# Kernel optimization log

Hardware: AMD Instinct MI355X
Metric: run time of the kernel (lower is better)

## Reference

```python
import jax, jax.numpy as jnp
import numpy as np

VOCAB = 16000   # code_size
EMBED = 16
HID = 256
B, T = 64, 128


def _glorot(key, shape, fan):
    return jax.random.normal(key, shape, dtype=jnp.float32) / np.sqrt(fan)


def setup_inputs() -> dict:
    key = jax.random.key(0)
    ks = jax.random.split(key, 20)
    inp = {
        "tokens": jax.random.randint(ks[0], (B, T), 0, VOCAB),
        "h0": jax.random.normal(ks[1], (B, HID), dtype=jnp.float32),
        "c0": jax.random.normal(ks[2], (B, HID), dtype=jnp.float32),
        "emb": jax.random.normal(ks[3], (VOCAB, EMBED), dtype=jnp.float32),
        # LSTMCell params, PyTorch layout: W_ih [4H, in], W_hh [4H, H], biases [4H]
        "Wih1": _glorot(ks[4], (4 * HID, EMBED), EMBED),
        "Whh1": _glorot(ks[5], (4 * HID, HID), HID),
        "bih1": jnp.zeros((4 * HID,), jnp.float32),
        "bhh1": jnp.zeros((4 * HID,), jnp.float32),
        "Wih2": _glorot(ks[6], (4 * HID, HID), HID),
        "Whh2": _glorot(ks[7], (4 * HID, HID), HID),
        "bih2": jnp.zeros((4 * HID,), jnp.float32),
        "bhh2": jnp.zeros((4 * HID,), jnp.float32),
        "Wih3": _glorot(ks[8], (4 * HID, HID), HID),
        "Whh3": _glorot(ks[9], (4 * HID, HID), HID),
        "bih3": jnp.zeros((4 * HID,), jnp.float32),
        "bhh3": jnp.zeros((4 * HID,), jnp.float32),
        # head: Linear(HID,HID) -> ReLU -> Linear(HID,VOCAB)
        "W1": _glorot(ks[10], (HID, HID), HID),
        "b1": jnp.zeros((HID,), jnp.float32),
        "W2": _glorot(ks[11], (VOCAB, HID), HID),
        "b2": jnp.zeros((VOCAB,), jnp.float32),
    }
    return inp


def _lstm_cell(x, h, c, Wih, Whh, bih, bhh):
    # PyTorch LSTMCell gate order: i, f, g, o
    gates = x @ Wih.T + bih + h @ Whh.T + bhh          # [B, 4H]
    i, f, g, o = jnp.split(gates, 4, axis=-1)
    i, f, o = jax.nn.sigmoid(i), jax.nn.sigmoid(f), jax.nn.sigmoid(o)
    g = jnp.tanh(g)
    c_new = f * c + i * g
    h_new = o * jnp.tanh(c_new)
    return h_new, c_new


def reference(tokens, h0, c0, emb,
              Wih1, Whh1, bih1, bhh1,
              Wih2, Whh2, bih2, bhh2,
              Wih3, Whh3, bih3, bhh3,
              W1, b1, W2, b2):
    Bn, Tn = tokens.shape
    x = emb[tokens]                       # [B, T, E]
    xs = jnp.swapaxes(x, 0, 1)            # [T, B, E] for scan over time

    def step(carry, x_t):
        h1, c1, h2, c2, h3, c3 = carry
        h1, c1 = _lstm_cell(x_t, h1, c1, Wih1, Whh1, bih1, bhh1)
        h2, c2 = _lstm_cell(h1, h2, c2, Wih2, Whh2, bih2, bhh2)
        h3, c3 = _lstm_cell(h2, h3, c3, Wih3, Whh3, bih3, bhh3)
        score = jax.nn.relu(h3 @ W1.T + b1) @ W2.T + b2   # [B, V]
        return (h1, c1, h2, c2, h3, c3), score

    init = (h0, c0, h0, c0, h0, c0)       # hidden1 = hidden2 = hidden3 = hidden
    _, scores = jax.lax.scan(step, init, xs)              # [T, B, V]
    scores = jnp.swapaxes(scores, 0, 1).reshape(Bn * Tn, -1)
    labels = tokens.reshape(-1)
    return scores, labels
```

## Files before the change

kernel.cpp:

```cpp
#include <hip/hip_runtime.h>
#include <hip/hip_bf16.h>
#include <stdint.h>

#define T_SEQ 128
#define BATCH 64
#define HIDN  256
#define EMB   16
#define VOCAB 16000

typedef __attribute__((ext_vector_type(8))) short short8v;
typedef __attribute__((ext_vector_type(4))) float f32x4;
typedef __attribute__((ext_vector_type(4))) unsigned short us4v;
typedef unsigned short ushort_t;
typedef unsigned long long u64_t;

#define OFF_WC1    0
#define OFF_WC2    131072
#define OFF_WC3    393216
#define OFF_BS2    655360
#define OFF_BS3    656384
#define OFF_FLAGS  657408
#define OFF_W1T    658432
#define OFF_H3     723968
#define OFF_S1     2821120
#define OFF_W2BF   3869696

#define OUT_XG     0
#define OUT_RINGS  8388608

#define RING_STRIDE 2113536
#define SLOT 16384

__device__ __forceinline__ ushort_t f2bf(float x) {
    __hip_bfloat16 h = __float2bfloat16(x);
    return *reinterpret_cast<ushort_t*>(&h);
}

__device__ __forceinline__ f32x4 sig4(f32x4 x) {
    f32x4 r;
    r[0] = __builtin_amdgcn_rcpf(1.f + __expf(-x[0]));
    r[1] = __builtin_amdgcn_rcpf(1.f + __expf(-x[1]));
    r[2] = __builtin_amdgcn_rcpf(1.f + __expf(-x[2]));
    r[3] = __builtin_amdgcn_rcpf(1.f + __expf(-x[3]));
    return r;
}
__device__ __forceinline__ f32x4 tanh4(f32x4 x) {
    f32x4 r;
    r[0] = 1.f - 2.f * __builtin_amdgcn_rcpf(1.f + __expf(2.f * x[0]));
    r[1] = 1.f - 2.f * __builtin_amdgcn_rcpf(1.f + __expf(2.f * x[1]));
    r[2] = 1.f - 2.f * __builtin_amdgcn_rcpf(1.f + __expf(2.f * x[2]));
    r[3] = 1.f - 2.f * __builtin_amdgcn_rcpf(1.f + __expf(2.f * x[3]));
    return r;
}
__device__ __forceinline__ f32x4 sx4(f32x4 v, int m) {
    f32x4 r;
    r[0] = __shfl_xor(v[0], m); r[1] = __shfl_xor(v[1], m);
    r[2] = __shfl_xor(v[2], m); r[3] = __shfl_xor(v[3], m);
    return r;
}
__device__ __forceinline__ void spin_ge(const int* p, int target) {
    while (__hip_atomic_load(p, __ATOMIC_RELAXED, __HIP_MEMORY_SCOPE_AGENT) < target) {}
}

__global__ void k_reset_flags(float* wsf) {
    ((int*)(wsf + OFF_FLAGS))[threadIdx.x] = 0;
}

__global__ void k_reorder_w(const float* __restrict__ Whh1,
                            const float* __restrict__ Wih2, const float* __restrict__ Whh2,
                            const float* __restrict__ Wih3, const float* __restrict__ Whh3,
                            float* __restrict__ wsf) {
    int bid = blockIdx.x;
    int layer = bid >> 10, c = bid & 1023;
    int wgi = c >> 7, rr = c & 127, jl = rr >> 2, gg = rr & 3;
    int row = gg * 256 + wgi * 32 + jl;
    int tid = threadIdx.x;
    if (layer == 0) {
        ushort_t* dst = (ushort_t*)(wsf + OFF_WC1) + (size_t)c * 256;
        dst[tid] = f2bf(Whh1[row * 256 + tid]);
    } else {
        const float* Wi = (layer == 1) ? Wih2 : Wih3;
        const float* Wh = (layer == 1) ? Whh2 : Whh3;
        ushort_t* dst = (ushort_t*)(wsf + ((layer == 1) ? OFF_WC2 : OFF_WC3)) + (size_t)c * 512;
        for (int k = tid; k < 512; k += 256)
            dst[k] = f2bf(k < 256 ? Wi[row * 256 + k] : Wh[row * 256 + k - 256]);
    }
}

__global__ void k_bias23(const float* __restrict__ bi2, const float* __restrict__ bh2,
                         const float* __restrict__ bi3, const float* __restrict__ bh3,
                         float* __restrict__ wsf) {
    int idx = blockIdx.x * 256 + threadIdx.x;
    int layer = idx >> 10, c = idx & 1023;
    int wgi = c >> 7, rr = c & 127, jl = rr >> 2, gg = rr & 3;
    int row = gg * 256 + wgi * 32 + jl;
    wsf[((layer == 0) ? OFF_BS2 : OFF_BS3) + c] =
        (layer == 0) ? (bi2[row] + bh2[row]) : (bi3[row] + bh3[row]);
}

__global__ void k_xg(const int* __restrict__ tokens, const float* __restrict__ emb,
                     const float* __restrict__ Wih1, const float* __restrict__ bih1,
                     const float* __restrict__ bhh1, float* __restrict__ xg) {
    int t = blockIdx.x, cg = blockIdx.y;
    int tid = threadIdx.x;
    __shared__ float xs[64][16];
    for (int idx = tid; idx < 1024; idx += 256) {
        int b = idx >> 4, e = idx & 15;
        xs[b][e] = emb[(size_t)tokens[b * T_SEQ + t] * 16 + e];
    }
    __syncthreads();
    int c = cg * 64 + (tid & 63);
    int b0 = (tid >> 6) * 16;
    int wgi = c >> 7, rr = c & 127, jl = rr >> 2, gg = rr & 3;
    int row = gg * 256 + wgi * 32 + jl;
    float wv[16];
    #pragma unroll
    for (int e = 0; e < 16; ++e) wv[e] = Wih1[row * 16 + e];
    float bias = bih1[row] + bhh1[row];
    float* dst = xg + ((size_t)t * 1024 + c) * 64 + b0;
    for (int b = 0; b < 16; ++b) {
        float s = bias;
        #pragma unroll
        for (int e = 0; e < 16; ++e) s += xs[b0 + b][e] * wv[e];
        dst[b] = s;
    }
}

__global__ void k_init_rings(const float* __restrict__ h0, ushort_t* __restrict__ rbase) {
    int idx = blockIdx.x * 256 + threadIdx.x;
    ushort_t v = f2bf(h0[idx]);
    rbase[idx] = v;
    rbase[RING_STRIDE + idx] = v;
    rbase[2 * RING_STRIDE + idx] = v;
}

__global__ void k_transpose_w1(const float* __restrict__ src, float* __restrict__ dst) {
    int idx = blockIdx.x * 256 + threadIdx.x;
    int n = idx & 255, k = idx >> 8;
    dst[idx] = src[n * 256 + k];
}

__global__ void k_conv_w2(const float* __restrict__ src, ushort_t* __restrict__ dst, int n) {
    int idx = blockIdx.x * 256 + threadIdx.x;
    if (idx < n) dst[idx] = f2bf(src[idx]);
}

template<int LAYER, int NKS>
__device__ __forceinline__ void lstm_body(
    int wg, int tid, const float* __restrict__ c0,
    float* __restrict__ wsf, float* __restrict__ outf,
    ushort_t* hA, ushort_t* hB, ushort_t* hS) {
    const int w = tid >> 6, lane = tid & 63, lr = lane & 15, lg = lane >> 4;
    const int g = lr & 3;
    const int K = NKS * 32;
    const ushort_t* WC = (const ushort_t*)(wsf + (LAYER == 0 ? OFF_WC1 : LAYER == 1 ? OFF_WC2 : OFF_WC3));
    int* fl = (int*)(wsf + OFF_FLAGS);
    float* H3 = wsf + OFF_H3;
    const float* xg = outf + OUT_XG;
    ushort_t* rbase = (ushort_t*)(outf + OUT_RINGS);
    ushort_t* ringIn = rbase + (size_t)(LAYER == 0 ? 0 : LAYER - 1) * RING_STRIDE;
    ushort_t* ringOwn = rbase + (size_t)LAYER * RING_STRIDE;

    const int ccol = wg * 128 + 2 * w * 16 + lr;
    short8v wr0[NKS], wr1[NKS];
    #pragma unroll
    for (int ks = 0; ks < NKS; ++ks) {
        wr0[ks] = *(const short8v*)(WC + (size_t)ccol * K + ks * 32 + lg * 8);
        wr1[ks] = *(const short8v*)(WC + (size_t)(ccol + 16) * K + ks * 32 + lg * 8);
    }
    float bs0 = 0.f, bs1 = 0.f;
    if (LAYER > 0) {
        const float* BS = wsf + (LAYER == 1 ? OFF_BS2 : OFF_BS3);
        bs0 = BS[ccol]; bs1 = BS[ccol + 16];
    }
    const int jj0 = w * 8 + (lr >> 2);
    const int j0 = wg * 32 + jj0;
    f32x4 cst[4][2];
    #pragma unroll
    for (int i = 0; i < 4; ++i)
        #pragma unroll
        for (int r = 0; r < 4; ++r) {
            cst[i][0][r] = c0[(i * 16 + lg * 4 + r) * 256 + j0];
            cst[i][1][r] = c0[(i * 16 + lg * 4 + r) * 256 + j0 + 4];
        }

    for (int t = 0; t < T_SEQ; ++t) {
        f32x4 xpre[8];
        if (LAYER == 0) {
            const float* xt = xg + ((size_t)t * 1024 + wg * 128) * 64;
            #pragma unroll
            for (int i = 0; i < 4; ++i) {
                xpre[i]     = *(const f32x4*)(xt + (size_t)(2 * w * 16 + lr) * 64 + i * 16 + lg * 4);
                xpre[i + 4] = *(const f32x4*)(xt + (size_t)((2 * w + 1) * 16 + lr) * 64 + i * 16 + lg * 4);
            }
        }
        if (LAYER == 0) {
            if (tid < 8) spin_ge(&fl[tid], t);
        } else {
            if (tid < 16) {
                int idx = tid & 7;
                const int* p = (tid < 8) ? &fl[(LAYER - 1) * 8 + idx] : &fl[LAYER * 8 + idx];
                spin_ge(p, (tid < 8) ? t + 1 : t);
            }
        }
        __syncthreads();
        {
            const u64_t* sA = (const u64_t*)(LAYER == 0 ? (ringOwn + (size_t)t * SLOT)
                                                        : (ringIn + (size_t)(t + 1) * SLOT));
            u64_t ta[16], tb[16];
            #pragma unroll
            for (int it = 0; it < 16; ++it)
                ta[it] = __hip_atomic_load(sA + it * 256 + tid, __ATOMIC_RELAXED, __HIP_MEMORY_SCOPE_AGENT);
            if (LAYER > 0) {
                const u64_t* sB = (const u64_t*)(ringOwn + (size_t)t * SLOT);
                #pragma unroll
                for (int it = 0; it < 16; ++it)
                    tb[it] = __hip_atomic_load(sB + it * 256 + tid, __ATOMIC_RELAXED, __HIP_MEMORY_SCOPE_AGENT);
            }
            #pragma unroll
            for (int it = 0; it < 16; ++it) {
                int e8 = it * 256 + tid;
                int row = e8 >> 6, c8 = e8 & 63, c16 = c8 >> 1;
                int off = row * 512 + (((c16 ^ (row & 7)) << 4) | ((c8 & 1) << 3));
                *(u64_t*)((char*)hA + off) = ta[it];
                if (LAYER > 0) *(u64_t*)((char*)hB + off) = tb[it];
            }
        }
        __syncthreads();
        f32x4 acc[4][2];
        if (LAYER == 0) {
            #pragma unroll
            for (int i = 0; i < 4; ++i) { acc[i][0] = xpre[i]; acc[i][1] = xpre[i + 4]; }
        } else {
            #pragma unroll
            for (int i = 0; i < 4; ++i) {
                acc[i][0] = (f32x4){bs0, bs0, bs0, bs0};
                acc[i][1] = (f32x4){bs1, bs1, bs1, bs1};
            }
        }
        #pragma unroll
        for (int i = 0; i < 4; ++i) {
            #pragma unroll
            for (int ks = 0; ks < NKS; ++ks) {
                const ushort_t* hsrc = (ks < 8) ? hA : hB;
                const int krem = ks & 7;
                short8v a = *(const short8v*)((const char*)hsrc + (i * 16 + lr) * 512 +
                                              (((krem * 4 + lg) ^ (lr & 7)) << 4));
                acc[i][0] = __builtin_amdgcn_mfma_f32_16x16x32_bf16(a, wr0[ks], acc[i][0], 0, 0, 0);
                acc[i][1] = __builtin_amdgcn_mfma_f32_16x16x32_bf16(a, wr1[ks], acc[i][1], 0, 0, 0);
            }
        }
        #pragma unroll
        for (int i = 0; i < 4; ++i) {
            #pragma unroll
            for (int f = 0; f < 2; ++f) {
                f32x4 av = acc[i][f];
                f32x4 act = (g == 2) ? tanh4(av) : sig4(av);
                f32x4 q1 = sx4(act, 1), q2 = sx4(act, 2), q3 = sx4(q2, 1);
                f32x4 gI = (g == 0) ? act : (g == 1) ? q1 : (g == 2) ? q2 : q3;
                f32x4 gF = (g == 1) ? act : (g == 0) ? q1 : (g == 3) ? q2 : q3;
                f32x4 gG = (g == 2) ? act : (g == 3) ? q1 : (g == 0) ? q2 : q3;
                f32x4 gO = (g == 3) ? act : (g == 2) ? q1 : (g == 1) ? q2 : q3;
                f32x4 cv = gF * cst[i][f] + gI * gG;
                cst[i][f] = cv;
                f32x4 hv = gO * tanh4(cv);
                float hval = (g == 0) ? hv[0] : (g == 1) ? hv[1] : (g == 2) ? hv[2] : hv[3];
                int brow = i * 16 + lg * 4 + g;
                int jj = jj0 + f * 4;
                hS[brow * 32 + jj] = f2bf(hval);
                if (LAYER == 2) H3[((size_t)brow * 128 + t) * 256 + wg * 32 + jj] = hval;
            }
        }
        __syncthreads();
        {
            u64_t* d8 = (u64_t*)(ringOwn + (size_t)(t + 1) * SLOT);
            #pragma unroll
            for (int it = 0; it < 2; ++it) {
                int e8 = it * 256 + tid;
                int row = e8 >> 3, c8 = e8 & 7;
                u64_t v = *(const u64_t*)(hS + row * 32 + c8 * 4);
                __hip_atomic_store(d8 + row * 64 + wg * 8 + c8, v, __ATOMIC_RELAXED, __HIP_MEMORY_SCOPE_AGENT);
            }
        }
        asm volatile("s_waitcnt vmcnt(0)" ::: "memory");
        __syncthreads();
        if (tid == 0)
            __hip_atomic_store(&fl[LAYER * 8 + wg], t + 1, __ATOMIC_RELAXED, __HIP_MEMORY_SCOPE_AGENT);
    }
}

__global__ __launch_bounds__(256, 1) void k_lstm(const float* __restrict__ c0,
                                                 float* __restrict__ wsf,
                                                 float* __restrict__ outf) {
    __shared__ __align__(16) ushort_t hA[16384];
    __shared__ __align__(16) ushort_t hB[16384];
    __shared__ __align__(16) ushort_t hS[2048];
    int layer = blockIdx.x >> 3, wg = blockIdx.x & 7;
    if (layer == 0)      lstm_body<0, 8>(wg, threadIdx.x, c0, wsf, outf, hA, hB, hS);
    else if (layer == 1) lstm_body<1, 16>(wg, threadIdx.x, c0, wsf, outf, hA, hB, hS);
    else                 lstm_body<2, 16>(wg, threadIdx.x, c0, wsf, outf, hA, hB, hS);
}

__global__ __launch_bounds__(256) void k_head1(const float* __restrict__ H3, const float* __restrict__ W1T,
                                               const float* __restrict__ b1, ushort_t* __restrict__ S1) {
    int tid = threadIdx.x;
    int r0 = blockIdx.x * 32;
    __shared__ float hs[32][256];
    {
        const f32x4* src = (const f32x4*)(H3 + (size_t)r0 * 256);
        f32x4* dstv = (f32x4*)hs;
        for (int i = tid; i < 32 * 64; i += 256) dstv[i] = src[i];
    }
    __syncthreads();
    int c0i = (tid & 63) * 4;
    int rg = (tid >> 6) * 8;
    f32x4 bias = *(const f32x4*)(b1 + c0i);
    f32x4 acc[8];
    #pragma unroll
    for (int r = 0; r < 8; ++r) acc[r] = bias;
    for (int k = 0; k < 256; ++k) {
        f32x4 wv = *(const f32x4*)(W1T + (size_t)k * 256 + c0i);
        #pragma unroll
        for (int r = 0; r < 8; ++r) acc[r] += hs[rg + r][k] * wv;
    }
    #pragma unroll
    for (int r = 0; r < 8; ++r) {
        int row = r0 + rg + r;
        f32x4 v = acc[r];
        us4v u;
        u.x = f2bf(fmaxf(v[0], 0.f));
        u.y = f2bf(fmaxf(v[1], 0.f));
        u.z = f2bf(fmaxf(v[2], 0.f));
        u.w = f2bf(fmaxf(v[3], 0.f));
        *(us4v*)(S1 + (size_t)row * 256 + c0i) = u;
    }
}

__global__ __launch_bounds__(256) void k_head2(const ushort_t* __restrict__ S1,
                                               const ushort_t* __restrict__ W2,
                                               const float* __restrict__ b2, float* __restrict__ out) {
    __shared__ __align__(16) ushort_t As[128][32];
    __shared__ __align__(16) ushort_t Bs[128][32];
    int tid = threadIdx.x;
    int n0 = blockIdx.x * 128;
    int m0 = blockIdx.y * 128;
    int wave = tid >> 6, lane = tid & 63;
    int lr = lane & 15, lg = lane >> 4;
    int wm = (wave >> 1) * 64, wn = (wave & 1) * 64;
    f32x4 acc[4][4] = {};

    for (int kk = 0; kk < 256; kk += 32) {
        int id = tid;
        #pragma unroll
        for (int rep = 0; rep < 2; ++rep, id += 256) {
            int r = id >> 2, ch = (id & 3) * 8;
            *(short8v*)(&As[r][ch]) = *(const short8v*)(S1 + (size_t)(m0 + r) * 256 + kk + ch);
            *(short8v*)(&Bs[r][ch]) = *(const short8v*)(W2 + (size_t)(n0 + r) * 256 + kk + ch);
        }
        __syncthreads();
        short8v a[4], bb[4];
        #pragma unroll
        for (int i = 0; i < 4; ++i) a[i]  = *(const short8v*)(&As[wm + i * 16 + lr][lg * 8]);
        #pragma unroll
        for (int i = 0; i < 4; ++i) bb[i] = *(const short8v*)(&Bs[wn + i * 16 + lr][lg * 8]);
        #pragma unroll
        for (int i = 0; i < 4; ++i)
            #pragma unroll
            for (int f = 0; f < 4; ++f)
                acc[i][f] = __builtin_amdgcn_mfma_f32_16x16x32_bf16(a[i], bb[f], acc[i][f], 0, 0, 0);
        __syncthreads();
    }
    #pragma unroll
    for (int f = 0; f < 4; ++f) {
        int col = n0 + wn + f * 16 + lr;
        float bias = b2[col];
        #pragma unroll
        for (int i = 0; i < 4; ++i) {
            int rowb = m0 + wm + i * 16 + lg * 4;
            #pragma unroll
            for (int r = 0; r < 4; ++r)
                out[(size_t)(rowb + r) * VOCAB + col] = acc[i][f][r] + bias;
        }
    }
}

__global__ void k_labels(const int* __restrict__ tokens, float* __restrict__ out) {
    int i = blockIdx.x * 256 + threadIdx.x;
    if (i < BATCH * T_SEQ) out[i] = (float)tokens[i];
}

extern "C" void kernel_launch(void* const* d_in, const int* in_sizes, int n_in,
                              void* d_out, int out_size, void* d_ws, size_t ws_size,
                              hipStream_t stream) {
    const int*   tokens = (const int*)d_in[0];
    const float* h0   = (const float*)d_in[1];
    const float* c0   = (const float*)d_in[2];
    const float* emb  = (const float*)d_in[3];
    const float* Wih1 = (const float*)d_in[4];
    const float* Whh1 = (const float*)d_in[5];
    const float* bih1 = (const float*)d_in[6];
    const float* bhh1 = (const float*)d_in[7];
    const float* Wih2 = (const float*)d_in[8];
    const float* Whh2 = (const float*)d_in[9];
    const float* bih2 = (const float*)d_in[10];
    const float* bhh2 = (const float*)d_in[11];
    const float* Wih3 = (const float*)d_in[12];
    const float* Whh3 = (const float*)d_in[13];
    const float* bih3 = (const float*)d_in[14];
    const float* bhh3 = (const float*)d_in[15];
    const float* W1   = (const float*)d_in[16];
    const float* b1   = (const float*)d_in[17];
    const float* W2   = (const float*)d_in[18];
    const float* b2   = (const float*)d_in[19];

    float* ws  = (float*)d_ws;
    float* out = (float*)d_out;

    k_reset_flags<<<1, 64, 0, stream>>>(ws);
    k_reorder_w<<<3072, 256, 0, stream>>>(Whh1, Wih2, Whh2, Wih3, Whh3, ws);
    k_bias23<<<8, 256, 0, stream>>>(bih2, bhh2, bih3, bhh3, ws);
    k_xg<<<dim3(128, 16), 256, 0, stream>>>(tokens, emb, Wih1, bih1, bhh1, out + OUT_XG);
    k_init_rings<<<64, 256, 0, stream>>>(h0, (ushort_t*)(out + OUT_RINGS));
    k_transpose_w1<<<256, 256, 0, stream>>>(W1, ws + OFF_W1T);
    k_conv_w2<<<16000, 256, 0, stream>>>(W2, (ushort_t*)(ws + OFF_W2BF), VOCAB * 256);

    k_lstm<<<24, 256, 0, stream>>>(c0, ws, out);

    k_head1<<<256, 256, 0, stream>>>(ws + OFF_H3, ws + OFF_W1T, b1, (ushort_t*)(ws + OFF_S1));
    dim3 g2(125, 64);
    k_head2<<<g2, 256, 0, stream>>>((const ushort_t*)(ws + OFF_S1),
                                    (const ushort_t*)(ws + OFF_W2BF), b2, out);
    k_labels<<<32, 256, 0, stream>>>(tokens, out + (size_t)BATCH * T_SEQ * VOCAB);
}
```

Before: 1.322 ms.

## Streamline LSTM recurrent step: 128-bit cache-bypass ring I/O, DPP shuffles, bf16 H3

```diff
diff --git a/kernel.cpp b/kernel.cpp
--- a/kernel.cpp
+++ b/kernel.cpp
@@ -7,6 +7,7 @@
 #define HIDN  256
 #define EMB   16
 #define VOCAB 16000
+#define HSTR  40
 
 typedef __attribute__((ext_vector_type(8))) short short8v;
 typedef __attribute__((ext_vector_type(4))) float f32x4;
@@ -36,30 +37,40 @@
     return *reinterpret_cast<ushort_t*>(&h);
 }
 
-__device__ __forceinline__ f32x4 sig4(f32x4 x) {
-    f32x4 r;
-    r[0] = __builtin_amdgcn_rcpf(1.f + __expf(-x[0]));
-    r[1] = __builtin_amdgcn_rcpf(1.f + __expf(-x[1]));
-    r[2] = __builtin_amdgcn_rcpf(1.f + __expf(-x[2]));
-    r[3] = __builtin_amdgcn_rcpf(1.f + __expf(-x[3]));
-    return r;
-}
-__device__ __forceinline__ f32x4 tanh4(f32x4 x) {
-    f32x4 r;
-    r[0] = 1.f - 2.f * __builtin_amdgcn_rcpf(1.f + __expf(2.f * x[0]));
-    r[1] = 1.f - 2.f * __builtin_amdgcn_rcpf(1.f + __expf(2.f * x[1]));
-    r[2] = 1.f - 2.f * __builtin_amdgcn_rcpf(1.f + __expf(2.f * x[2]));
-    r[3] = 1.f - 2.f * __builtin_amdgcn_rcpf(1.f + __expf(2.f * x[3]));
-    return r;
-}
-__device__ __forceinline__ f32x4 sx4(f32x4 v, int m) {
-    f32x4 r;
-    r[0] = __shfl_xor(v[0], m); r[1] = __shfl_xor(v[1], m);
-    r[2] = __shfl_xor(v[2], m); r[3] = __shfl_xor(v[3], m);
-    return r;
-}
+__device__ __forceinline__ float dpp_x1(float x) {
+    return __builtin_bit_cast(float, __builtin_amdgcn_mov_dpp(
+        __builtin_bit_cast(int, x), 0xB1, 0xF, 0xF, true));
+}
+__device__ __forceinline__ float dpp_x2(float x) {
+    return __builtin_bit_cast(float, __builtin_amdgcn_mov_dpp(
+        __builtin_bit_cast(int, x), 0x4E, 0xF, 0xF, true));
+}
+__device__ __forceinline__ f32x4 dpp4_x1(f32x4 v) {
+    f32x4 r; r[0]=dpp_x1(v[0]); r[1]=dpp_x1(v[1]); r[2]=dpp_x1(v[2]); r[3]=dpp_x1(v[3]); return r;
+}
+__device__ __forceinline__ f32x4 dpp4_x2(f32x4 v) {
+    f32x4 r; r[0]=dpp_x2(v[0]); r[1]=dpp_x2(v[1]); r[2]=dpp_x2(v[2]); r[3]=dpp_x2(v[3]); return r;
+}
+
 __device__ __forceinline__ void spin_ge(const int* p, int target) {
     while (__hip_atomic_load(p, __ATOMIC_RELAXED, __HIP_MEMORY_SCOPE_AGENT) < target) {}
+}
+
+__device__ __forceinline__ f32x4 bypass_ld128(const void* p) {
+    f32x4 v;
+    asm volatile("global_load_dwordx4 %0, %1, off sc0 sc1" : "=v"(v) : "v"((uint64_t)p));
+    return v;
+}
+__device__ __forceinline__ void bypass_st128(void* p, f32x4 v) {
+    asm volatile("global_store_dwordx4 %0, %1, off sc0 sc1" :: "v"((uint64_t)p), "v"(v) : "memory");
+}
+__device__ __forceinline__ void vm_drain() {
+    asm volatile("s_waitcnt vmcnt(0)" ::: "memory");
+    __builtin_amdgcn_sched_barrier(0);
+}
+__device__ __forceinline__ void lgkm_drain() {
+    asm volatile("s_waitcnt lgkmcnt(0)" ::: "memory");
+    __builtin_amdgcn_sched_barrier(0);
 }
 
 __global__ void k_reset_flags(float* wsf) {
@@ -155,7 +166,7 @@
     const int K = NKS * 32;
     const ushort_t* WC = (const ushort_t*)(wsf + (LAYER == 0 ? OFF_WC1 : LAYER == 1 ? OFF_WC2 : OFF_WC3));
     int* fl = (int*)(wsf + OFF_FLAGS);
-    float* H3 = wsf + OFF_H3;
+    ushort_t* H3b = (ushort_t*)(wsf + OFF_H3);
     const float* xg = outf + OUT_XG;
     ushort_t* rbase = (ushort_t*)(outf + OUT_RINGS);
     ushort_t* ringIn = rbase + (size_t)(LAYER == 0 ? 0 : LAYER - 1) * RING_STRIDE;
@@ -183,6 +194,10 @@
             cst[i][0][r] = c0[(i * 16 + lg * 4 + r) * 256 + j0];
             cst[i][1][r] = c0[(i * 16 + lg * 4 + r) * 256 + j0 + 4];
         }
+
+    const float sOwn = (g == 2) ? 2.f : -1.f;
+    const float aOwn = (g == 2) ? -2.f : 1.f;
+    const float bOwn = (g == 2) ? 1.f : 0.f;
 
     for (int t = 0; t < T_SEQ; ++t) {
         f32x4 xpre[8];
@@ -205,25 +220,26 @@
         }
         __syncthreads();
         {
-            const u64_t* sA = (const u64_t*)(LAYER == 0 ? (ringOwn + (size_t)t * SLOT)
-                                                        : (ringIn + (size_t)(t + 1) * SLOT));
-            u64_t ta[16], tb[16];
-            #pragma unroll
-            for (int it = 0; it < 16; ++it)
-                ta[it] = __hip_atomic_load(sA + it * 256 + tid, __ATOMIC_RELAXED, __HIP_MEMORY_SCOPE_AGENT);
+            const char* sA = (const char*)(LAYER == 0 ? (ringOwn + (size_t)t * SLOT)
+                                                      : (ringIn + (size_t)(t + 1) * SLOT));
+            f32x4 ta[8], tb[8];
+            #pragma unroll
+            for (int it = 0; it < 8; ++it)
+                ta[it] = bypass_ld128(sA + it * 4096 + tid * 16);
             if (LAYER > 0) {
-                const u64_t* sB = (const u64_t*)(ringOwn + (size_t)t * SLOT);
+                const char* sB = (const char*)(ringOwn + (size_t)t * SLOT);
                 #pragma unroll
-                for (int it = 0; it < 16; ++it)
-                    tb[it] = __hip_atomic_load(sB + it * 256 + tid, __ATOMIC_RELAXED, __HIP_MEMORY_SCOPE_AGENT);
-            }
-            #pragma unroll
-            for (int it = 0; it < 16; ++it) {
-                int e8 = it * 256 + tid;
-                int row = e8 >> 6, c8 = e8 & 63, c16 = c8 >> 1;
-                int off = row * 512 + (((c16 ^ (row & 7)) << 4) | ((c8 & 1) << 3));
-                *(u64_t*)((char*)hA + off) = ta[it];
-                if (LAYER > 0) *(u64_t*)((char*)hB + off) = tb[it];
+                for (int it = 0; it < 8; ++it)
+                    tb[it] = bypass_ld128(sB + it * 4096 + tid * 16);
+            }
+            vm_drain();
+            #pragma unroll
+            for (int it = 0; it < 8; ++it) {
+                int e16 = it * 256 + tid;
+                int row = e16 >> 5, c16 = e16 & 31;
+                int off = row * 512 + ((c16 ^ (row & 15)) << 4);
+                *(f32x4*)((char*)hA + off) = ta[it];
+                if (LAYER > 0) *(f32x4*)((char*)hB + off) = tb[it];
             }
         }
         __syncthreads();
@@ -245,7 +261,7 @@
                 const ushort_t* hsrc = (ks < 8) ? hA : hB;
                 const int krem = ks & 7;
                 short8v a = *(const short8v*)((const char*)hsrc + (i * 16 + lr) * 512 +
-                                              (((krem * 4 + lg) ^ (lr & 7)) << 4));
+                                              (((krem * 4 + lg) ^ lr) << 4));
                 acc[i][0] = __builtin_amdgcn_mfma_f32_16x16x32_bf16(a, wr0[ks], acc[i][0], 0, 0, 0);
                 acc[i][1] = __builtin_amdgcn_mfma_f32_16x16x32_bf16(a, wr1[ks], acc[i][1], 0, 0, 0);
             }
@@ -255,34 +271,36 @@
             #pragma unroll
             for (int f = 0; f < 2; ++f) {
                 f32x4 av = acc[i][f];
-                f32x4 act = (g == 2) ? tanh4(av) : sig4(av);
-                f32x4 q1 = sx4(act, 1), q2 = sx4(act, 2), q3 = sx4(q2, 1);
+                f32x4 act;
+                #pragma unroll
+                for (int r = 0; r < 4; ++r) {
+                    float e = __expf(sOwn * av[r]);
+                    act[r] = fmaf(aOwn, __builtin_amdgcn_rcpf(1.f + e), bOwn);
+                }
+                f32x4 q1 = dpp4_x1(act), q2 = dpp4_x2(act), q3 = dpp4_x1(q2);
                 f32x4 gI = (g == 0) ? act : (g == 1) ? q1 : (g == 2) ? q2 : q3;
                 f32x4 gF = (g == 1) ? act : (g == 0) ? q1 : (g == 3) ? q2 : q3;
                 f32x4 gG = (g == 2) ? act : (g == 3) ? q1 : (g == 0) ? q2 : q3;
                 f32x4 gO = (g == 3) ? act : (g == 2) ? q1 : (g == 1) ? q2 : q3;
                 f32x4 cv = gF * cst[i][f] + gI * gG;
                 cst[i][f] = cv;
-                f32x4 hv = gO * tanh4(cv);
-                float hval = (g == 0) ? hv[0] : (g == 1) ? hv[1] : (g == 2) ? hv[2] : hv[3];
+                float cg = (g == 0) ? cv[0] : (g == 1) ? cv[1] : (g == 2) ? cv[2] : cv[3];
+                float go = (g == 0) ? gO[0] : (g == 1) ? gO[1] : (g == 2) ? gO[2] : gO[3];
+                float e2 = __expf(2.f * cg);
+                float th = fmaf(-2.f, __builtin_amdgcn_rcpf(1.f + e2), 1.f);
+                float hval = go * th;
                 int brow = i * 16 + lg * 4 + g;
-                int jj = jj0 + f * 4;
-                hS[brow * 32 + jj] = f2bf(hval);
-                if (LAYER == 2) H3[((size_t)brow * 128 + t) * 256 + wg * 32 + jj] = hval;
-            }
-        }
-        __syncthreads();
+                hS[brow * HSTR + jj0 + f * 4] = f2bf(hval);
+            }
+        }
+        lgkm_drain();
         {
-            u64_t* d8 = (u64_t*)(ringOwn + (size_t)(t + 1) * SLOT);
-            #pragma unroll
-            for (int it = 0; it < 2; ++it) {
-                int e8 = it * 256 + tid;
-                int row = e8 >> 3, c8 = e8 & 7;
-                u64_t v = *(const u64_t*)(hS + row * 32 + c8 * 4);
-                __hip_atomic_store(d8 + row * 64 + wg * 8 + c8, v, __ATOMIC_RELAXED, __HIP_MEMORY_SCOPE_AGENT);
-            }
-        }
-        asm volatile("s_waitcnt vmcnt(0)" ::: "memory");
+            f32x4 hv4 = *(const f32x4*)((const char*)hS + lane * (HSTR * 2) + w * 16);
+            bypass_st128(ringOwn + (size_t)(t + 1) * SLOT + (size_t)lane * 256 + wg * 32 + w * 8, hv4);
+            if (LAYER == 2)
+                *(f32x4*)(H3b + (((size_t)lane * 128 + t) * 256 + wg * 32 + w * 8)) = hv4;
+        }
+        vm_drain();
         __syncthreads();
         if (tid == 0)
             __hip_atomic_store(&fl[LAYER * 8 + wg], t + 1, __ATOMIC_RELAXED, __HIP_MEMORY_SCOPE_AGENT);
@@ -294,22 +312,29 @@
                                                  float* __restrict__ outf) {
     __shared__ __align__(16) ushort_t hA[16384];
     __shared__ __align__(16) ushort_t hB[16384];
-    __shared__ __align__(16) ushort_t hS[2048];
+    __shared__ __align__(16) ushort_t hS[64 * HSTR];
     int layer = blockIdx.x >> 3, wg = blockIdx.x & 7;
     if (layer == 0)      lstm_body<0, 8>(wg, threadIdx.x, c0, wsf, outf, hA, hB, hS);
     else if (layer == 1) lstm_body<1, 16>(wg, threadIdx.x, c0, wsf, outf, hA, hB, hS);
     else                 lstm_body<2, 16>(wg, threadIdx.x, c0, wsf, outf, hA, hB, hS);
 }
 
-__global__ __launch_bounds__(256) void k_head1(const float* __restrict__ H3, const float* __restrict__ W1T,
+__global__ __launch_bounds__(256) void k_head1(const ushort_t* __restrict__ H3, const float* __restrict__ W1T,
                                                const float* __restrict__ b1, ushort_t* __restrict__ S1) {
     int tid = threadIdx.x;
     int r0 = blockIdx.x * 32;
     __shared__ float hs[32][256];
     {
-        const f32x4* src = (const f32x4*)(H3 + (size_t)r0 * 256);
-        f32x4* dstv = (f32x4*)hs;
-        for (int i = tid; i < 32 * 64; i += 256) dstv[i] = src[i];
+        const short8v* src = (const short8v*)(H3 + (size_t)r0 * 256);
+        float* hsf = &hs[0][0];
+        for (int i = tid; i < 1024; i += 256) {
+            short8v v = src[i];
+            #pragma unroll
+            for (int e = 0; e < 8; ++e) {
+                unsigned int u = (unsigned int)(unsigned short)v[e];
+                hsf[i * 8 + e] = __uint_as_float(u << 16);
+            }
+        }
     }
     __syncthreads();
     int c0i = (tid & 63) * 4;
@@ -426,7 +451,7 @@
 
     k_lstm<<<24, 256, 0, stream>>>(c0, ws, out);
 
-    k_head1<<<256, 256, 0, stream>>>(ws + OFF_H3, ws + OFF_W1T, b1, (ushort_t*)(ws + OFF_S1));
+    k_head1<<<256, 256, 0, stream>>>((const ushort_t*)(ws + OFF_H3), ws + OFF_W1T, b1, (ushort_t*)(ws + OFF_S1));
     dim3 g2(125, 64);
     k_head2<<<g2, 256, 0, stream>>>((const ushort_t*)(ws + OFF_S1),
                                     (const ushort_t*)(ws + OFF_W2BF), b2, out);
```

Result: faster. 1.192 ms (-9.9%).
